# Performance work log

Measured on AMD Instinct MI355X. Metric: run time of the kernel, lower is better.

## Reference

```python
import jax, jax.numpy as jnp
from jax import lax
import numpy as np

N_T = 70            # linspace(0, 60, 70) RK4 grid
STATE_DIM = 12
NOISE_STD = 0.01
T0 = jnp.linspace(0.0, 60.0, N_T)
DEFAULT_TIMES = jnp.array([0, 2, 4, 6, 8, 10, 12, 14, 16, 18, 20, 25, 30, 40, 50, 60], dtype=jnp.float32)
EPORA_DATA = jnp.array([0.01713, 0.145, 0.2442, 0.7659, 1.0, 0.8605, 0.7829, 0.5705,
                        0.6217, 0.331, 0.3388, 0.3116, 0.05062, 0.02504, 0.01163, 0.01163], dtype=jnp.float32)
PARAM_SHIFT = jnp.array([0.5, 0.05, 4.0], dtype=jnp.float32)
PARAM_SCALE = jnp.array([2.5, 0.15, 6.0], dtype=jnp.float32)


def _deriv(x, k1, k2, tau, E):
    # x: [B, 12]; k1,k2,tau: [B]; E: scalar EpoRA(t)
    x1, x2, x3 = x[:, 0], x[:, 1], x[:, 2]
    q1, q2, q3, q4, q5, q6, q7, out = (x[:, 4], x[:, 5], x[:, 6], x[:, 7],
                                       x[:, 8], x[:, 9], x[:, 10], x[:, 11])
    r = 8.0 / tau
    return jnp.stack([
        -k1 * x1 * E + k2 * out,
        -x2 * x2 + k1 * x1 * E,
        -k2 * x3 + x2 * x2,
        -k2 * out + k2 * x3,
        r * (x3 - q1),
        r * (q1 - q2),
        r * (q2 - q3),
        r * (q3 - q4),
        r * (q4 - q5),
        r * (q5 - q6),
        r * (q6 - q7),
        r * (q7 - out),
    ], axis=1)


def _simulate(ps):
    # ps: [B, 3] transformed parameters -> trajectory [N_T, B, 12]
    B = ps.shape[0]
    k1, k2, tau = ps[:, 0], ps[:, 1], ps[:, 2]
    dt = T0[1] - T0[0]
    t_start = T0[:-1]
    # EpoRA is a function of t only: precompute at the 3 RK4 stage times per step
    e_lo = jnp.interp(t_start, DEFAULT_TIMES, EPORA_DATA)
    e_mid = jnp.interp(t_start + 0.5 * dt, DEFAULT_TIMES, EPORA_DATA)
    e_hi = jnp.interp(t_start + dt, DEFAULT_TIMES, EPORA_DATA)
    x0 = jnp.zeros((B, STATE_DIM), dtype=ps.dtype).at[:, 0].set(3.71)

    def step(x, es):
        ea, eb, ec = es
        s1 = _deriv(x, k1, k2, tau, ea)
        s2 = _deriv(x + 0.5 * dt * s1, k1, k2, tau, eb)
        s3 = _deriv(x + 0.5 * dt * s2, k1, k2, tau, eb)
        s4 = _deriv(x + dt * s3, k1, k2, tau, ec)
        xn = x + (dt / 6.0) * (s1 + 2.0 * s2 + 2.0 * s3 + s4)
        return xn, xn

    _, traj = lax.scan(step, x0, (e_lo, e_mid, e_hi))
    return jnp.concatenate([x0[None], traj], axis=0)  # [70, B, 12]


def _forward(parameters, design):
    ps = PARAM_SHIFT + jax.scipy.stats.norm.cdf(parameters) * PARAM_SCALE  # [B,3]
    sol = _simulate(ps)                                   # [70, B, 12]
    y1 = 0.33 * (sol[:, :, 1] + sol[:, :, 2]).T           # [B, 70]
    y2 = 0.26 * (sol[:, :, 0] + sol[:, :, 1] + sol[:, :, 2]).T
    interp = jax.vmap(lambda yb: jnp.interp(design, T0, yb))
    return jnp.concatenate([interp(y1), interp(y2)], axis=1)  # [B, 2*obs_dim]


def setup_inputs() -> dict:
    key = jax.random.key(0)
    k1, k2, k3 = jax.random.split(key, 3)
    B, OBS = 65536, 8
    parameters = jax.random.normal(k1, (B, 3), dtype=jnp.float32)
    design = jnp.sort(60.0 * jax.random.uniform(k2, (OBS,), dtype=jnp.float32))
    noise = jax.random.normal(k3, (B, 2 * OBS), dtype=jnp.float32)
    return {"parameters": parameters, "design": design, "noise": noise}


def reference(parameters, design, noise):
    true_obs = _forward(parameters, design)
    noised_obs = true_obs + NOISE_STD * noise
    return true_obs, noised_obs
```

## Files before the change

kernel.cpp:

```cpp
#include <hip/hip_runtime.h>
#include <math.h>

#define NSTEP 69
#define OBS 8
#define NSTATE 11

namespace {

constexpr float kDT = 60.0f / 69.0f;

struct ETab { float lo[NSTEP]; float mid[NSTEP]; float hi[NSTEP]; };

constexpr float interp_e(float t) {
    constexpr float DTm[16] = {0.f,2.f,4.f,6.f,8.f,10.f,12.f,14.f,16.f,18.f,20.f,25.f,30.f,40.f,50.f,60.f};
    constexpr float EP[16]  = {0.01713f,0.145f,0.2442f,0.7659f,1.0f,0.8605f,0.7829f,0.5705f,
                               0.6217f,0.331f,0.3388f,0.3116f,0.05062f,0.02504f,0.01163f,0.01163f};
    if (t >= 60.0f) return EP[15];
    if (t <= 0.0f)  return EP[0];
    int k = 0;
    for (int m = 0; m < 15; m++) if (t >= DTm[m]) k = m;
    float u = (t - DTm[k]) / (DTm[k + 1] - DTm[k]);
    return EP[k] + u * (EP[k + 1] - EP[k]);
}

constexpr ETab make_etab() {
    ETab e{};
    for (int s = 0; s < NSTEP; s++) {
        float t0 = (float)s * kDT;
        e.lo[s]  = interp_e(t0);
        e.mid[s] = interp_e(t0 + 0.5f * kDT);
        e.hi[s]  = interp_e(t0 + kDT);
    }
    return e;
}

}

__device__ constexpr ETab ETAB = make_etab();

__device__ __forceinline__ void deriv(const float (&xs)[NSTATE], float k1, float k2,
                                      float r, float E, float (&d)[NSTATE]) {
    float a  = k1 * xs[0] * E;
    float sq = xs[1] * xs[1];
    d[0] = fmaf(k2, xs[10], -a);
    d[1] = a - sq;
    d[2] = fmaf(-k2, xs[2], sq);
    #pragma unroll
    for (int i = 3; i < NSTATE; i++) d[i] = r * (xs[i - 1] - xs[i]);
}

__global__ __launch_bounds__(256) void stats5_kernel(
    const float* __restrict__ params,
    const float* __restrict__ design,
    const float* __restrict__ noise,
    float* __restrict__ out,
    int B)
{
    int b = blockIdx.x * blockDim.x + threadIdx.x;
    if (b >= B) return;

    int   ij[OBS]; float wj[OBS], w1j[OBS];
    #pragma unroll
    for (int j = 0; j < OBS; j++) {
        float pos = design[j] * (1.0f / kDT);
        int i = (int)pos;
        i = i < 0 ? 0 : (i > NSTEP - 1 ? NSTEP - 1 : i);
        float w = pos - (float)i;
        ij[j]  = __builtin_amdgcn_readfirstlane(i);
        int wb = __builtin_amdgcn_readfirstlane(__float_as_int(w));
        wj[j]  = __int_as_float(wb);
        w1j[j] = 1.0f - wj[j];
    }

    float p0 = params[3 * b], p1 = params[3 * b + 1], p2 = params[3 * b + 2];
    const float INV_SQRT2 = 0.7071067811865476f;
    float k1  = fmaf(0.5f * erfcf(-p0 * INV_SQRT2), 2.5f,  0.5f);
    float k2  = fmaf(0.5f * erfcf(-p1 * INV_SQRT2), 0.15f, 0.05f);
    float tau = fmaf(0.5f * erfcf(-p2 * INV_SQRT2), 6.0f,  4.0f);
    float r = 8.0f / tau;

    float o1[OBS], o2[OBS];
    #pragma unroll
    for (int j = 0; j < OBS; j++) { o1[j] = 0.f; o2[j] = 0.f; }

    float x[NSTATE];
    #pragma unroll
    for (int i = 0; i < NSTATE; i++) x[i] = 0.f;
    x[0] = 3.71f;

    {
        float y1 = 0.33f * (x[1] + x[2]);
        float y2 = 0.26f * (x[0] + x[1] + x[2]);
        #pragma unroll
        for (int j = 0; j < OBS; j++) {
            if (0 == ij[j]) { o1[j] += w1j[j] * y1; o2[j] += w1j[j] * y2; }
        }
    }

    for (int s = 0; s < NSTEP; s++) {
        float ea = ETAB.lo[s], eb = ETAB.mid[s], ec = ETAB.hi[s];
        float d1[NSTATE], d2[NSTATE], d3[NSTATE], d4[NSTATE], xs[NSTATE];
        deriv(x, k1, k2, r, ea, d1);
        #pragma unroll
        for (int i = 0; i < NSTATE; i++) xs[i] = fmaf(0.5f * kDT, d1[i], x[i]);
        deriv(xs, k1, k2, r, eb, d2);
        #pragma unroll
        for (int i = 0; i < NSTATE; i++) xs[i] = fmaf(0.5f * kDT, d2[i], x[i]);
        deriv(xs, k1, k2, r, eb, d3);
        #pragma unroll
        for (int i = 0; i < NSTATE; i++) xs[i] = fmaf(kDT, d3[i], x[i]);
        deriv(xs, k1, k2, r, ec, d4);
        #pragma unroll
        for (int i = 0; i < NSTATE; i++)
            x[i] = fmaf(kDT * (1.0f / 6.0f), d1[i] + 2.0f * (d2[i] + d3[i]) + d4[i], x[i]);

        float y1 = 0.33f * (x[1] + x[2]);
        float y2 = 0.26f * (x[0] + x[1] + x[2]);
        int ti = s + 1;
        #pragma unroll
        for (int j = 0; j < OBS; j++) {
            if (ti == ij[j])     { o1[j] += w1j[j] * y1; o2[j] += w1j[j] * y2; }
            if (ti == ij[j] + 1) { o1[j] += wj[j]  * y1; o2[j] += wj[j]  * y2; }
        }
    }

    long long base = (long long)b * 16;
    long long nb   = (long long)B * 16;
    #pragma unroll
    for (int j = 0; j < OBS; j++) {
        float t1 = o1[j], t2 = o2[j];
        out[base + j]          = t1;
        out[base + 8 + j]      = t2;
        out[nb + base + j]     = fmaf(0.01f, noise[base + j],     t1);
        out[nb + base + 8 + j] = fmaf(0.01f, noise[base + 8 + j], t2);
    }
}

extern "C" void kernel_launch(void* const* d_in, const int* in_sizes, int n_in,
                              void* d_out, int out_size, void* d_ws, size_t ws_size,
                              hipStream_t stream) {
    const float* params = (const float*)d_in[0];
    const float* design = (const float*)d_in[1];
    const float* noise  = (const float*)d_in[2];
    float* out = (float*)d_out;
    int B = in_sizes[0] / 3;
    int block = 256;
    int grid = (B + block - 1) / block;
    stats5_kernel<<<grid, block, 0, stream>>>(params, design, noise, out, B);
}
```

Measured before the change: 98.92 us.

## Pack RK4 delay chain into float2 vectors and defer observation interpolation

The eight delay-chain states are packed into float2 vectors so the compiler can emit packed FP32 ops, and k1*E is precomputed once per stage. Observation sampling now uses a bitmask of the needed time indices, stores raw state snapshots, and applies the interpolation weights and output scaling once after the loop. Output and noise traffic move to float4 vector loads and stores. The aim is to cut VALU instruction count in the compute-bound RK4 loop, at the cost of relying on the compiler to actually produce packed FP32 instructions.

```diff
diff --git a/kernel.cpp b/kernel.cpp
--- a/kernel.cpp
+++ b/kernel.cpp
@@ -3,7 +3,8 @@
 
 #define NSTEP 69
 #define OBS 8
-#define NSTATE 11
+
+typedef float f32x2 __attribute__((ext_vector_type(2)));
 
 namespace {
 
@@ -38,15 +39,34 @@
 
 __device__ constexpr ETab ETAB = make_etab();
 
-__device__ __forceinline__ void deriv(const float (&xs)[NSTATE], float k1, float k2,
-                                      float r, float E, float (&d)[NSTATE]) {
-    float a  = k1 * xs[0] * E;
-    float sq = xs[1] * xs[1];
-    d[0] = fmaf(k2, xs[10], -a);
-    d[1] = a - sq;
-    d[2] = fmaf(-k2, xs[2], sq);
-    #pragma unroll
-    for (int i = 3; i < NSTATE; i++) d[i] = r * (xs[i - 1] - xs[i]);
+struct St { float x0, x1, x2; f32x2 P0, P1, P2, P3; };
+struct Dv { float d0, d1, d2; f32x2 D0, D1, D2, D3; };
+
+__device__ __forceinline__ Dv deriv(const St& s, float k1E, float k2, f32x2 r2) {
+    Dv d;
+    float a  = k1E * s.x0;
+    float sq = s.x1 * s.x1;
+    d.d0 = fmaf(k2, s.P3.y, -a);
+    d.d1 = a - sq;
+    d.d2 = fmaf(-k2, s.x2, sq);
+    f32x2 s0; s0.x = s.x2; s0.y = s.P3.x;
+    d.D0 = r2 * (s0   - s.P0);
+    d.D1 = r2 * (s.P0 - s.P1);
+    d.D2 = r2 * (s.P1 - s.P2);
+    d.D3 = r2 * (s.P2 - s.P3);
+    return d;
+}
+
+__device__ __forceinline__ St axpy(const St& x, float c, const Dv& d) {
+    St y; f32x2 c2 = {c, c};
+    y.x0 = fmaf(c, d.d0, x.x0);
+    y.x1 = fmaf(c, d.d1, x.x1);
+    y.x2 = fmaf(c, d.d2, x.x2);
+    y.P0 = c2 * d.D0 + x.P0;
+    y.P1 = c2 * d.D1 + x.P1;
+    y.P2 = c2 * d.D2 + x.P2;
+    y.P3 = c2 * d.D3 + x.P3;
+    return y;
 }
 
 __global__ __launch_bounds__(256) void stats5_kernel(
@@ -59,7 +79,7 @@
     int b = blockIdx.x * blockDim.x + threadIdx.x;
     if (b >= B) return;
 
-    int   ij[OBS]; float wj[OBS], w1j[OBS];
+    int ij[OBS], ij1[OBS]; float wj[OBS], w1j[OBS];
     #pragma unroll
     for (int j = 0; j < OBS; j++) {
         float pos = design[j] * (1.0f / kDT);
@@ -67,9 +87,17 @@
         i = i < 0 ? 0 : (i > NSTEP - 1 ? NSTEP - 1 : i);
         float w = pos - (float)i;
         ij[j]  = __builtin_amdgcn_readfirstlane(i);
+        ij1[j] = ij[j] + 1;
         int wb = __builtin_amdgcn_readfirstlane(__float_as_int(w));
         wj[j]  = __int_as_float(wb);
         w1j[j] = 1.0f - wj[j];
+    }
+
+    unsigned long long m_lo = 0ull, m_hi = 0ull;
+    #pragma unroll
+    for (int j = 0; j < OBS; j++) {
+        if (ij[j]  < 64) m_lo |= 1ull << ij[j];  else m_hi |= 1ull << (ij[j]  - 64);
+        if (ij1[j] < 64) m_lo |= 1ull << ij1[j]; else m_hi |= 1ull << (ij1[j] - 64);
     }
 
     float p0 = params[3 * b], p1 = params[3 * b + 1], p2 = params[3 * b + 2];
@@ -78,62 +106,87 @@
     float k2  = fmaf(0.5f * erfcf(-p1 * INV_SQRT2), 0.15f, 0.05f);
     float tau = fmaf(0.5f * erfcf(-p2 * INV_SQRT2), 6.0f,  4.0f);
     float r = 8.0f / tau;
-
-    float o1[OBS], o2[OBS];
-    #pragma unroll
-    for (int j = 0; j < OBS; j++) { o1[j] = 0.f; o2[j] = 0.f; }
-
-    float x[NSTATE];
-    #pragma unroll
-    for (int i = 0; i < NSTATE; i++) x[i] = 0.f;
-    x[0] = 3.71f;
-
-    {
-        float y1 = 0.33f * (x[1] + x[2]);
-        float y2 = 0.26f * (x[0] + x[1] + x[2]);
+    f32x2 r2 = {r, r};
+
+    float a12[OBS], a0[OBS], b12[OBS], b0[OBS];
+    #pragma unroll
+    for (int j = 0; j < OBS; j++) { a12[j] = 0.f; a0[j] = 0.f; b12[j] = 0.f; b0[j] = 0.f; }
+
+    St x;
+    x.x0 = 3.71f; x.x1 = 0.f; x.x2 = 0.f;
+    x.P0 = (f32x2){0.f, 0.f}; x.P1 = x.P0; x.P2 = x.P0; x.P3 = x.P0;
+
+    if (m_lo & 1ull) {
         #pragma unroll
-        for (int j = 0; j < OBS; j++) {
-            if (0 == ij[j]) { o1[j] += w1j[j] * y1; o2[j] += w1j[j] * y2; }
-        }
+        for (int j = 0; j < OBS; j++)
+            if (ij[j] == 0) { a12[j] = 0.f; a0[j] = 3.71f; }
     }
 
     for (int s = 0; s < NSTEP; s++) {
         float ea = ETAB.lo[s], eb = ETAB.mid[s], ec = ETAB.hi[s];
-        float d1[NSTATE], d2[NSTATE], d3[NSTATE], d4[NSTATE], xs[NSTATE];
-        deriv(x, k1, k2, r, ea, d1);
-        #pragma unroll
-        for (int i = 0; i < NSTATE; i++) xs[i] = fmaf(0.5f * kDT, d1[i], x[i]);
-        deriv(xs, k1, k2, r, eb, d2);
-        #pragma unroll
-        for (int i = 0; i < NSTATE; i++) xs[i] = fmaf(0.5f * kDT, d2[i], x[i]);
-        deriv(xs, k1, k2, r, eb, d3);
-        #pragma unroll
-        for (int i = 0; i < NSTATE; i++) xs[i] = fmaf(kDT, d3[i], x[i]);
-        deriv(xs, k1, k2, r, ec, d4);
-        #pragma unroll
-        for (int i = 0; i < NSTATE; i++)
-            x[i] = fmaf(kDT * (1.0f / 6.0f), d1[i] + 2.0f * (d2[i] + d3[i]) + d4[i], x[i]);
-
-        float y1 = 0.33f * (x[1] + x[2]);
-        float y2 = 0.26f * (x[0] + x[1] + x[2]);
+        float k1a = k1 * ea, k1b = k1 * eb, k1c = k1 * ec;
+
+        Dv d1 = deriv(x, k1a, k2, r2);
+        St t  = axpy(x, 0.5f * kDT, d1);
+        Dv d2 = deriv(t, k1b, k2, r2);
+        t     = axpy(x, 0.5f * kDT, d2);
+        Dv d3 = deriv(t, k1b, k2, r2);
+        t     = axpy(x, kDT, d3);
+        Dv d4 = deriv(t, k1c, k2, r2);
+
+        const float c6 = kDT * (1.0f / 6.0f);
+        {
+            float u;
+            u = fmaf(2.0f, d2.d0 + d3.d0, d1.d0 + d4.d0); x.x0 = fmaf(c6, u, x.x0);
+            u = fmaf(2.0f, d2.d1 + d3.d1, d1.d1 + d4.d1); x.x1 = fmaf(c6, u, x.x1);
+            u = fmaf(2.0f, d2.d2 + d3.d2, d1.d2 + d4.d2); x.x2 = fmaf(c6, u, x.x2);
+            f32x2 two = {2.0f, 2.0f}, c62 = {c6, c6}, v;
+            v = two * (d2.D0 + d3.D0) + (d1.D0 + d4.D0); x.P0 = c62 * v + x.P0;
+            v = two * (d2.D1 + d3.D1) + (d1.D1 + d4.D1); x.P1 = c62 * v + x.P1;
+            v = two * (d2.D2 + d3.D2) + (d1.D2 + d4.D2); x.P2 = c62 * v + x.P2;
+            v = two * (d2.D3 + d3.D3) + (d1.D3 + d4.D3); x.P3 = c62 * v + x.P3;
+        }
+
         int ti = s + 1;
-        #pragma unroll
-        for (int j = 0; j < OBS; j++) {
-            if (ti == ij[j])     { o1[j] += w1j[j] * y1; o2[j] += w1j[j] * y2; }
-            if (ti == ij[j] + 1) { o1[j] += wj[j]  * y1; o2[j] += wj[j]  * y2; }
+        bool any = (ti < 64) ? ((m_lo >> ti) & 1ull) : ((m_hi >> (ti - 64)) & 1ull);
+        if (any) {
+            float s12 = x.x1 + x.x2;
+            #pragma unroll
+            for (int j = 0; j < OBS; j++) {
+                if (ti == ij[j])  { a12[j] = s12; a0[j] = x.x0; }
+                if (ti == ij1[j]) { b12[j] = s12; b0[j] = x.x0; }
+            }
         }
+    }
+
+    float o1[OBS], o2[OBS];
+    #pragma unroll
+    for (int j = 0; j < OBS; j++) {
+        o1[j] = 0.33f * fmaf(w1j[j], a12[j], wj[j] * b12[j]);
+        o2[j] = 0.26f * fmaf(w1j[j], a0[j] + a12[j], wj[j] * (b0[j] + b12[j]));
     }
 
     long long base = (long long)b * 16;
     long long nb   = (long long)B * 16;
-    #pragma unroll
-    for (int j = 0; j < OBS; j++) {
-        float t1 = o1[j], t2 = o2[j];
-        out[base + j]          = t1;
-        out[base + 8 + j]      = t2;
-        out[nb + base + j]     = fmaf(0.01f, noise[base + j],     t1);
-        out[nb + base + 8 + j] = fmaf(0.01f, noise[base + 8 + j], t2);
-    }
+    float4* outv = (float4*)(out + base);
+    float4* outn = (float4*)(out + nb + base);
+    const float4* nz = (const float4*)(noise + base);
+
+    float4 v0 = make_float4(o1[0], o1[1], o1[2], o1[3]);
+    float4 v1 = make_float4(o1[4], o1[5], o1[6], o1[7]);
+    float4 v2 = make_float4(o2[0], o2[1], o2[2], o2[3]);
+    float4 v3 = make_float4(o2[4], o2[5], o2[6], o2[7]);
+    outv[0] = v0; outv[1] = v1; outv[2] = v2; outv[3] = v3;
+
+    float4 n0 = nz[0], n1 = nz[1], n2 = nz[2], n3 = nz[3];
+    outn[0] = make_float4(fmaf(0.01f, n0.x, v0.x), fmaf(0.01f, n0.y, v0.y),
+                          fmaf(0.01f, n0.z, v0.z), fmaf(0.01f, n0.w, v0.w));
+    outn[1] = make_float4(fmaf(0.01f, n1.x, v1.x), fmaf(0.01f, n1.y, v1.y),
+                          fmaf(0.01f, n1.z, v1.z), fmaf(0.01f, n1.w, v1.w));
+    outn[2] = make_float4(fmaf(0.01f, n2.x, v2.x), fmaf(0.01f, n2.y, v2.y),
+                          fmaf(0.01f, n2.z, v2.z), fmaf(0.01f, n2.w, v2.w));
+    outn[3] = make_float4(fmaf(0.01f, n3.x, v3.x), fmaf(0.01f, n3.y, v3.y),
+                          fmaf(0.01f, n3.z, v3.z), fmaf(0.01f, n3.w, v3.w));
 }
 
 extern "C" void kernel_launch(void* const* d_in, const int* in_sizes, int n_in,
```

Measured after the change: 87.97 us. -11.1%, faster.
